# Kernel tuning notes

Measured on AMD Instinct MI355X. Metric: run time of the kernel, lower is better.

The kernel has to match this reference:

```python
import jax, jax.numpy as jnp
import numpy as np

EMBED = 1024
HEAD = 128

def setup_inputs() -> dict:
    key = jax.random.key(0)
    k1, k2, k3, k4 = jax.random.split(key, 4)
    x = jax.random.normal(k1, (8, 2048, EMBED), dtype=jnp.float32)
    s = 1.0 / np.sqrt(EMBED)
    Wk = jax.random.normal(k2, (EMBED, HEAD), dtype=jnp.float32) * s
    Wq = jax.random.normal(k3, (EMBED, HEAD), dtype=jnp.float32) * s
    Wv = jax.random.normal(k4, (EMBED, HEAD), dtype=jnp.float32) * s
    return {"x": x, "Wk": Wk, "Wq": Wq, "Wv": Wv}

def reference(x, Wk, Wq, Wv):
    # x: [B,T,E]; projections: [B,T,H]
    k = x @ Wk
    q = x @ Wq
    v = x @ Wv
    T = x.shape[1]
    # NOTE: original scales by 1/sqrt(embedding_size), not head_size
    scale = 1.0 / jnp.sqrt(jnp.asarray(EMBED, dtype=x.dtype))
    scores = jnp.einsum('bth,bsh->bts', q, k) * scale  # [B,T,T]
    causal = jnp.tril(jnp.ones((T, T), dtype=bool))
    scores = jnp.where(causal, scores, -jnp.inf)
    attn = jax.nn.softmax(scores, axis=-1)
    return jnp.einsum('bts,bsh->bth', attn, v)
```

## Files before the change

kernel.cpp:

```cpp
#include <hip/hip_runtime.h>
#include <math.h>

typedef short bf16x2 __attribute__((ext_vector_type(2)));
typedef short bf16x4 __attribute__((ext_vector_type(4)));
typedef short bf16x8 __attribute__((ext_vector_type(8)));
typedef float f32x4 __attribute__((ext_vector_type(4)));

#define EMBED 1024
#define HEAD 128
#define BATCH 8
#define SEQ 2048

__device__ __forceinline__ short f2bf(float f) {
  union { float f; unsigned u; } v;
  v.f = f;
  unsigned r = v.u + 0x7fffu + ((v.u >> 16) & 1u);
  return (short)(r >> 16);
}

__device__ __forceinline__ void async_copy16(const void* g, void* l) {
#if __has_builtin(__builtin_amdgcn_global_load_lds)
  __builtin_amdgcn_global_load_lds(
      (const __attribute__((address_space(1))) unsigned int*)g,
      (__attribute__((address_space(3))) unsigned int*)l, 16, 0, 0);
#else
  *(f32x4*)l = *(const f32x4*)g;
#endif
}

__global__ __launch_bounds__(256) void wtrans_kernel(
    const float* __restrict__ Wq, const float* __restrict__ Wk,
    const float* __restrict__ Wv, short* __restrict__ WT) {
  __shared__ float tile[32][33];
  int kt = blockIdx.x * 32;
  int ht = blockIdx.y * 32;
  int mtx = blockIdx.z;
  const float* W = (mtx == 0) ? Wq : ((mtx == 1) ? Wk : Wv);
  float scale = (mtx == 0) ? (1.4426950408889634f / 32.0f) : 1.0f;
  int tc = threadIdx.x & 31;
  int tr = threadIdx.x >> 5;
#pragma unroll
  for (int i = 0; i < 4; i++) {
    int r = tr + i * 8;
    tile[r][tc] = W[(size_t)(kt + r) * HEAD + ht + tc];
  }
  __syncthreads();
#pragma unroll
  for (int i = 0; i < 4; i++) {
    int r = tr + i * 8;
    WT[(size_t)(mtx * HEAD + ht + r) * EMBED + kt + tc] = f2bf(tile[tc][r] * scale);
  }
}

__global__ __launch_bounds__(512, 2) void proj_kernel(
    const float* __restrict__ x, const short* __restrict__ WT,
    short* __restrict__ q, short* __restrict__ k, short* __restrict__ vT) {
  __shared__ __align__(16) short As[2][64 * 72];
  __shared__ __align__(16) short Bs[2][3072 * 8];
  int tid = threadIdx.x;
  int w = tid >> 6, lane = tid & 63, quad = lane >> 4, sub = lane & 15;
  int mw = w & 1, nw = w >> 1;
  int mt = blockIdx.x;
  int m0 = mt * 64;
  int bb = m0 >> 11;
  int t0 = m0 & 2047;

  int arow = tid >> 3;
  int akq = (tid & 7) * 8;
  const float* xbase = x + (size_t)(m0 + arow) * EMBED + akq;
  int aoff = arow * 72 + akq;

  int kcg = tid >> 7;
  int n0 = tid & 127;
  const short* wsrc[6];
  int bdst[6];
#pragma unroll
  for (int j = 0; j < 3; j++)
#pragma unroll
    for (int kk = 0; kk < 2; kk++) {
      int kc = kcg * 2 + kk;
      int n = j * 128 + n0;
      wsrc[j * 2 + kk] = WT + (size_t)n * EMBED + kc * 8;
      bdst[j * 2 + kk] = (kc * 384 + n) * 8;
    }

  f32x4 acc[2][6];
#pragma unroll
  for (int am = 0; am < 2; am++)
#pragma unroll
    for (int an = 0; an < 6; an++) acc[am][an] = (f32x4)(0.0f);

  {
    f32x4 x0 = *(const f32x4*)(xbase + 0);
    f32x4 x1 = *(const f32x4*)(xbase + 4);
    bf16x8 w0;
    w0[0]=f2bf(x0[0]); w0[1]=f2bf(x0[1]); w0[2]=f2bf(x0[2]); w0[3]=f2bf(x0[3]);
    w0[4]=f2bf(x1[0]); w0[5]=f2bf(x1[1]); w0[6]=f2bf(x1[2]); w0[7]=f2bf(x1[3]);
    *(bf16x8*)&As[0][aoff] = w0;
#pragma unroll
    for (int j = 0; j < 6; j++) async_copy16(wsrc[j], &Bs[0][bdst[j]]);
  }
  f32x4 xr0 = *(const f32x4*)(xbase + 64);
  f32x4 xr1 = *(const f32x4*)(xbase + 68);

  for (int it = 0; it < 16; it++) {
    int cur = it & 1;
    __syncthreads();
    if (it < 15) {
      int nxt = cur ^ 1;
      bf16x8 w0;
      w0[0]=f2bf(xr0[0]); w0[1]=f2bf(xr0[1]); w0[2]=f2bf(xr0[2]); w0[3]=f2bf(xr0[3]);
      w0[4]=f2bf(xr1[0]); w0[5]=f2bf(xr1[1]); w0[6]=f2bf(xr1[2]); w0[7]=f2bf(xr1[3]);
      *(bf16x8*)&As[nxt][aoff] = w0;
      int kb1 = (it + 1) * 64;
#pragma unroll
      for (int j = 0; j < 6; j++)
        async_copy16(wsrc[j] + kb1, &Bs[nxt][bdst[j]]);
      if (it < 14) {
        int kb2 = (it + 2) * 64;
        xr0 = *(const f32x4*)(xbase + kb2);
        xr1 = *(const f32x4*)(xbase + kb2 + 4);
      }
    }
#pragma unroll
    for (int ks = 0; ks < 2; ks++) {
      bf16x8 a0 = *(const bf16x8*)&As[cur][(mw * 32 + sub) * 72 + ks * 32 + quad * 8];
      bf16x8 a1 = *(const bf16x8*)&As[cur][(mw * 32 + 16 + sub) * 72 + ks * 32 + quad * 8];
#pragma unroll
      for (int an = 0; an < 6; an++) {
        bf16x8 bf = *(const bf16x8*)&Bs[cur][((ks * 4 + quad) * 384 + nw * 96 + an * 16 + sub) * 8];
        acc[0][an] = __builtin_amdgcn_mfma_f32_16x16x32_bf16(a0, bf, acc[0][an], 0, 0, 0);
        acc[1][an] = __builtin_amdgcn_mfma_f32_16x16x32_bf16(a1, bf, acc[1][an], 0, 0, 0);
      }
    }
  }

  __syncthreads();
  short* vls = &As[0][0];
#pragma unroll
  for (int am = 0; am < 2; am++)
#pragma unroll
    for (int an = 0; an < 6; an++) {
      int g = nw * 6 + an;
      int mtx = g >> 3;
      int colm = (g & 7) * 16 + sub;
      if (mtx < 2) {
        short* dst = (mtx == 0) ? q : k;
#pragma unroll
        for (int r = 0; r < 4; r++) {
          int m = m0 + mw * 32 + am * 16 + quad * 4 + r;
          dst[(size_t)m * HEAD + colm] = f2bf(acc[am][an][r]);
        }
      } else {
        int mm = mw * 32 + am * 16 + quad * 4;
        bf16x4 pv;
#pragma unroll
        for (int r = 0; r < 4; r++) pv[r] = f2bf(acc[am][an][r]);
        *(bf16x4*)&vls[colm * 72 + mm] = pv;
      }
    }
  __syncthreads();
  int h = tid >> 2, seg = tid & 3;
  bf16x8 v0 = *(const bf16x8*)&vls[h * 72 + seg * 16];
  bf16x8 v1 = *(const bf16x8*)&vls[h * 72 + seg * 16 + 8];
  short* dp = vT + (size_t)(bb * HEAD + h) * SEQ + t0 + seg * 16;
  *(bf16x8*)(dp) = v0;
  *(bf16x8*)(dp + 8) = v1;
}

__global__ __launch_bounds__(256, 4) void attn_kernel(
    const short* __restrict__ q, const short* __restrict__ k,
    const short* __restrict__ vT, float* __restrict__ o_acc,
    float* __restrict__ l_acc) {
  __shared__ __align__(16) short Kb[2][4096];
  __shared__ __align__(16) short Vb[2][4096];
  __shared__ __align__(16) short Pb[4][2][16 * 40];
  int tid = threadIdx.x;
  int w = tid >> 6, lane = tid & 63, quad = lane >> 4, sub = lane & 15;
  int bx = blockIdx.x;
  int b = bx & 7;
  int v = 79 - (bx >> 3);
  int qt, c;
  if (v < 8)       { qt = v;                               c = 0; }
  else if (v < 24) { int i2 = v - 8;  qt = 8  + (i2 >> 1); c = i2 & 1; }
  else if (v < 48) { int i2 = v - 24; qt = 16 + i2 / 3;    c = i2 % 3; }
  else             { int i2 = v - 48; qt = 24 + (i2 >> 2); c = i2 & 3; }
  int q0 = qt * 64;
  int kb0 = c * 512;
  int len = min(512, q0 + 64 - kb0);
  int ntiles = len >> 5;

  const short* kp = k + (size_t)b * SEQ * HEAD;
  const short* vp = vT + (size_t)b * HEAD * SEQ;
  int cc0 = tid, cc1 = tid + 256;

  bf16x8 qf[4];
  const short* qrow = q + (size_t)(b * SEQ + q0 + w * 16 + sub) * HEAD + quad * 8;
#pragma unroll
  for (int kc = 0; kc < 4; kc++) qf[kc] = *(const bf16x8*)(qrow + kc * 32);

  f32x4 o[8];
#pragma unroll
  for (int h = 0; h < 8; h++) o[h] = (f32x4)(0.0f);
  float l[4] = {0.0f, 0.0f, 0.0f, 0.0f};
  int wrow = q0 + w * 16;
  int qrq = wrow + quad * 4;

  async_copy16(kp + (size_t)(kb0 + (cc0 & 31)) * HEAD + (cc0 >> 5) * 8, &Kb[0][cc0 * 8]);
  async_copy16(kp + (size_t)(kb0 + (cc1 & 31)) * HEAD + (cc1 >> 5) * 8, &Kb[0][cc1 * 8]);
  async_copy16(vp + (size_t)(cc0 & 127) * SEQ + kb0 + (cc0 >> 7) * 8, &Vb[0][cc0 * 8]);
  async_copy16(vp + (size_t)(cc1 & 127) * SEQ + kb0 + (cc1 >> 7) * 8, &Vb[0][cc1 * 8]);

  for (int j = 0; j < ntiles; j++) {
    int kb = kb0 + j * 32;
    int cur = j & 1;
    __syncthreads();
    if (j + 1 < ntiles) {
      int nxt = cur ^ 1;
      int kb1 = kb + 32;
      async_copy16(kp + (size_t)(kb1 + (cc0 & 31)) * HEAD + (cc0 >> 5) * 8, &Kb[nxt][cc0 * 8]);
      async_copy16(kp + (size_t)(kb1 + (cc1 & 31)) * HEAD + (cc1 >> 5) * 8, &Kb[nxt][cc1 * 8]);
      async_copy16(vp + (size_t)(cc0 & 127) * SEQ + kb1 + (cc0 >> 7) * 8, &Vb[nxt][cc0 * 8]);
      async_copy16(vp + (size_t)(cc1 & 127) * SEQ + kb1 + (cc1 >> 7) * 8, &Vb[nxt][cc1 * 8]);
    }
    f32x4 s0 = (f32x4)(0.0f), s1 = (f32x4)(0.0f);
#pragma unroll
    for (int kk = 0; kk < 4; kk++) {
      bf16x8 f0 = *(const bf16x8*)&Kb[cur][((kk * 4 + quad) * 32 + sub) * 8];
      bf16x8 f1 = *(const bf16x8*)&Kb[cur][((kk * 4 + quad) * 32 + 16 + sub) * 8];
      s0 = __builtin_amdgcn_mfma_f32_16x16x32_bf16(qf[kk], f0, s0, 0, 0, 0);
      s1 = __builtin_amdgcn_mfma_f32_16x16x32_bf16(qf[kk], f1, s1, 0, 0, 0);
    }
    bool edge = (kb + 31 > wrow);
    float e0[4], e1[4];
#pragma unroll
    for (int r = 0; r < 4; r++) {
      e0[r] = __builtin_amdgcn_exp2f(s0[r]);
      e1[r] = __builtin_amdgcn_exp2f(s1[r]);
    }
    if (edge) {
#pragma unroll
      for (int r = 0; r < 4; r++) {
        if (kb + sub > qrq + r) e0[r] = 0.0f;
        if (kb + 16 + sub > qrq + r) e1[r] = 0.0f;
      }
    }
    short* pw = &Pb[w][cur][0];
#pragma unroll
    for (int r = 0; r < 4; r++) {
      l[r] += e0[r] + e1[r];
      pw[(quad * 4 + r) * 40 + sub] = f2bf(e0[r]);
      pw[(quad * 4 + r) * 40 + sub + 16] = f2bf(e1[r]);
    }
    bf16x8 pa = *(const bf16x8*)&pw[sub * 40 + quad * 8];
#pragma unroll
    for (int h8 = 0; h8 < 8; h8++) {
      bf16x8 vf = *(const bf16x8*)&Vb[cur][(quad * 128 + h8 * 16 + sub) * 8];
      o[h8] = __builtin_amdgcn_mfma_f32_16x16x32_bf16(pa, vf, o[h8], 0, 0, 0);
    }
  }

  float* ob = o_acc + (size_t)(b * SEQ + qrq) * HEAD + sub;
#pragma unroll
  for (int r = 0; r < 4; r++)
#pragma unroll
    for (int h8 = 0; h8 < 8; h8++)
      unsafeAtomicAdd(ob + (size_t)r * HEAD + h8 * 16, o[h8][r]);
#pragma unroll
  for (int r = 0; r < 4; r++) {
#pragma unroll
    for (int off = 1; off < 16; off <<= 1) l[r] += __shfl_xor(l[r], off);
  }
  if (sub == 0) {
#pragma unroll
    for (int r = 0; r < 4; r++)
      unsafeAtomicAdd(&l_acc[b * SEQ + qrq + r], l[r]);
  }
}

__global__ __launch_bounds__(256) void norm_kernel(
    float* __restrict__ o, const float* __restrict__ l_acc) {
  int idx = blockIdx.x * 256 + threadIdx.x;
  f32x4 v = ((const f32x4*)o)[idx];
  float inv = 1.0f / l_acc[idx >> 5];
  v[0] *= inv; v[1] *= inv; v[2] *= inv; v[3] *= inv;
  ((f32x4*)o)[idx] = v;
}

extern "C" void kernel_launch(void* const* d_in, const int* in_sizes, int n_in,
                              void* d_out, int out_size, void* d_ws, size_t ws_size,
                              hipStream_t stream) {
  const float* x  = (const float*)d_in[0];
  const float* Wk = (const float*)d_in[1];
  const float* Wq = (const float*)d_in[2];
  const float* Wv = (const float*)d_in[3];
  char* ws = (char*)d_ws;
  short* WT    = (short*)(ws);
  short* vT    = (short*)(ws + (size_t)1  * (1 << 20));
  short* q     = (short*)(ws + (size_t)5  * (1 << 20));
  short* k     = (short*)(ws + (size_t)9  * (1 << 20));
  float* l_acc = (float*)(ws + (size_t)13 * (1 << 20));
  float* out   = (float*)d_out;

  hipMemsetAsync(out, 0, (size_t)BATCH * SEQ * HEAD * sizeof(float), stream);
  hipMemsetAsync(l_acc, 0, (size_t)BATCH * SEQ * sizeof(float), stream);
  wtrans_kernel<<<dim3(32, 4, 3), 256, 0, stream>>>(Wq, Wk, Wv, WT);
  proj_kernel<<<dim3(256), 512, 0, stream>>>(x, WT, q, k, vT);
  attn_kernel<<<dim3(640), 256, 0, stream>>>(q, k, vT, out, l_acc);
  norm_kernel<<<dim3(2048), 256, 0, stream>>>(out, l_acc);
}
```

Before: 175.6 us.

## Store weights, K and V in LDS-tile-ordered global layouts for contiguous async copies

The weight pre-pass now writes the bf16 weights already in the shared-memory tile order used by the projection kernel. The projection kernel writes K and V directly in 32-key tile blocks matching the attention kernel's LDS layout, which removes the LDS transpose and extra syncs for V. Each async copy in both kernels then reads a fully contiguous 8 KB block instead of strided rows. The cost is scattered 2-byte stores for K in the projection epilogue and a more specialised, harder-to-reuse intermediate layout.

Result: faster. 156.7 us (-10.8%).

```diff
diff --git a/kernel.cpp b/kernel.cpp
--- a/kernel.cpp
+++ b/kernel.cpp
@@ -28,42 +28,31 @@
 #endif
 }
 
-__global__ __launch_bounds__(256) void wtrans_kernel(
+__global__ __launch_bounds__(384) void wtrans_kernel(
     const float* __restrict__ Wq, const float* __restrict__ Wk,
-    const float* __restrict__ Wv, short* __restrict__ WT) {
-  __shared__ float tile[32][33];
-  int kt = blockIdx.x * 32;
-  int ht = blockIdx.y * 32;
-  int mtx = blockIdx.z;
+    const float* __restrict__ Wv, short* __restrict__ WT3) {
+  int kc8 = blockIdx.x;
+  int n = threadIdx.x;
+  int mtx = n >> 7, h = n & 127;
   const float* W = (mtx == 0) ? Wq : ((mtx == 1) ? Wk : Wv);
   float scale = (mtx == 0) ? (1.4426950408889634f / 32.0f) : 1.0f;
-  int tc = threadIdx.x & 31;
-  int tr = threadIdx.x >> 5;
-#pragma unroll
-  for (int i = 0; i < 4; i++) {
-    int r = tr + i * 8;
-    tile[r][tc] = W[(size_t)(kt + r) * HEAD + ht + tc];
-  }
-  __syncthreads();
-#pragma unroll
-  for (int i = 0; i < 4; i++) {
-    int r = tr + i * 8;
-    WT[(size_t)(mtx * HEAD + ht + r) * EMBED + kt + tc] = f2bf(tile[tc][r] * scale);
-  }
+  bf16x8 o;
+#pragma unroll
+  for (int j = 0; j < 8; j++)
+    o[j] = f2bf(W[(size_t)(kc8 * 8 + j) * HEAD + h] * scale);
+  *(bf16x8*)&WT3[(size_t)kc8 * 3072 + n * 8] = o;
 }
 
 __global__ __launch_bounds__(512, 2) void proj_kernel(
-    const float* __restrict__ x, const short* __restrict__ WT,
-    short* __restrict__ q, short* __restrict__ k, short* __restrict__ vT) {
+    const float* __restrict__ x, const short* __restrict__ WT3,
+    short* __restrict__ q, short* __restrict__ kG, short* __restrict__ vG) {
   __shared__ __align__(16) short As[2][64 * 72];
-  __shared__ __align__(16) short Bs[2][3072 * 8];
+  __shared__ __align__(16) short Bs[2][24576];
   int tid = threadIdx.x;
   int w = tid >> 6, lane = tid & 63, quad = lane >> 4, sub = lane & 15;
   int mw = w & 1, nw = w >> 1;
   int mt = blockIdx.x;
   int m0 = mt * 64;
-  int bb = m0 >> 11;
-  int t0 = m0 & 2047;
 
   int arow = tid >> 3;
   int akq = (tid & 7) * 8;
@@ -72,17 +61,12 @@
 
   int kcg = tid >> 7;
   int n0 = tid & 127;
-  const short* wsrc[6];
   int bdst[6];
 #pragma unroll
   for (int j = 0; j < 3; j++)
 #pragma unroll
-    for (int kk = 0; kk < 2; kk++) {
-      int kc = kcg * 2 + kk;
-      int n = j * 128 + n0;
-      wsrc[j * 2 + kk] = WT + (size_t)n * EMBED + kc * 8;
-      bdst[j * 2 + kk] = (kc * 384 + n) * 8;
-    }
+    for (int kk = 0; kk < 2; kk++)
+      bdst[j * 2 + kk] = ((kcg * 2 + kk) * 384 + j * 128 + n0) * 8;
 
   f32x4 acc[2][6];
 #pragma unroll
@@ -98,7 +82,7 @@
     w0[4]=f2bf(x1[0]); w0[5]=f2bf(x1[1]); w0[6]=f2bf(x1[2]); w0[7]=f2bf(x1[3]);
     *(bf16x8*)&As[0][aoff] = w0;
 #pragma unroll
-    for (int j = 0; j < 6; j++) async_copy16(wsrc[j], &Bs[0][bdst[j]]);
+    for (int j = 0; j < 6; j++) async_copy16(WT3 + bdst[j], &Bs[0][bdst[j]]);
   }
   f32x4 xr0 = *(const f32x4*)(xbase + 64);
   f32x4 xr1 = *(const f32x4*)(xbase + 68);
@@ -112,10 +96,10 @@
       w0[0]=f2bf(xr0[0]); w0[1]=f2bf(xr0[1]); w0[2]=f2bf(xr0[2]); w0[3]=f2bf(xr0[3]);
       w0[4]=f2bf(xr1[0]); w0[5]=f2bf(xr1[1]); w0[6]=f2bf(xr1[2]); w0[7]=f2bf(xr1[3]);
       *(bf16x8*)&As[nxt][aoff] = w0;
-      int kb1 = (it + 1) * 64;
+      int bsrc = (it + 1) * 24576;
 #pragma unroll
       for (int j = 0; j < 6; j++)
-        async_copy16(wsrc[j] + kb1, &Bs[nxt][bdst[j]]);
+        async_copy16(WT3 + bsrc + bdst[j], &Bs[nxt][bdst[j]]);
       if (it < 14) {
         int kb2 = (it + 2) * 64;
         xr0 = *(const f32x4*)(xbase + kb2);
@@ -135,42 +119,36 @@
     }
   }
 
-  __syncthreads();
-  short* vls = &As[0][0];
 #pragma unroll
   for (int am = 0; am < 2; am++)
 #pragma unroll
     for (int an = 0; an < 6; an++) {
       int g = nw * 6 + an;
-      int mtx = g >> 3;
-      int colm = (g & 7) * 16 + sub;
-      if (mtx < 2) {
-        short* dst = (mtx == 0) ? q : k;
+      int hcol = (g & 7) * 16 + sub;
+      if (g < 8) {
 #pragma unroll
         for (int r = 0; r < 4; r++) {
           int m = m0 + mw * 32 + am * 16 + quad * 4 + r;
-          dst[(size_t)m * HEAD + colm] = f2bf(acc[am][an][r]);
+          q[(size_t)m * HEAD + hcol] = f2bf(acc[am][an][r]);
         }
+      } else if (g < 16) {
+        size_t base = (size_t)(mt * 2 + mw) * 4096 + (hcol >> 3) * 256 + (hcol & 7);
+#pragma unroll
+        for (int r = 0; r < 4; r++)
+          kG[base + (am * 16 + quad * 4 + r) * 8] = f2bf(acc[am][an][r]);
       } else {
-        int mm = mw * 32 + am * 16 + quad * 4;
         bf16x4 pv;
 #pragma unroll
         for (int r = 0; r < 4; r++) pv[r] = f2bf(acc[am][an][r]);
-        *(bf16x4*)&vls[colm * 72 + mm] = pv;
-      }
-    }
-  __syncthreads();
-  int h = tid >> 2, seg = tid & 3;
-  bf16x8 v0 = *(const bf16x8*)&vls[h * 72 + seg * 16];
-  bf16x8 v1 = *(const bf16x8*)&vls[h * 72 + seg * 16 + 8];
-  short* dp = vT + (size_t)(bb * HEAD + h) * SEQ + t0 + seg * 16;
-  *(bf16x8*)(dp) = v0;
-  *(bf16x8*)(dp + 8) = v1;
+        *(bf16x4*)&vG[(size_t)(mt * 2 + mw) * 4096 + (am * 2 + (quad >> 1)) * 1024 +
+                      hcol * 8 + (quad & 1) * 4] = pv;
+      }
+    }
 }
 
 __global__ __launch_bounds__(256, 4) void attn_kernel(
-    const short* __restrict__ q, const short* __restrict__ k,
-    const short* __restrict__ vT, float* __restrict__ o_acc,
+    const short* __restrict__ q, const short* __restrict__ kG,
+    const short* __restrict__ vG, float* __restrict__ o_acc,
     float* __restrict__ l_acc) {
   __shared__ __align__(16) short Kb[2][4096];
   __shared__ __align__(16) short Vb[2][4096];
@@ -190,8 +168,8 @@
   int len = min(512, q0 + 64 - kb0);
   int ntiles = len >> 5;
 
-  const short* kp = k + (size_t)b * SEQ * HEAD;
-  const short* vp = vT + (size_t)b * HEAD * SEQ;
+  const short* kp = kG + (size_t)b * SEQ * HEAD;
+  const short* vp = vG + (size_t)b * SEQ * HEAD;
   int cc0 = tid, cc1 = tid + 256;
 
   bf16x8 qf[4];
@@ -206,10 +184,13 @@
   int wrow = q0 + w * 16;
   int qrq = wrow + quad * 4;
 
-  async_copy16(kp + (size_t)(kb0 + (cc0 & 31)) * HEAD + (cc0 >> 5) * 8, &Kb[0][cc0 * 8]);
-  async_copy16(kp + (size_t)(kb0 + (cc1 & 31)) * HEAD + (cc1 >> 5) * 8, &Kb[0][cc1 * 8]);
-  async_copy16(vp + (size_t)(cc0 & 127) * SEQ + kb0 + (cc0 >> 7) * 8, &Vb[0][cc0 * 8]);
-  async_copy16(vp + (size_t)(cc1 & 127) * SEQ + kb0 + (cc1 >> 7) * 8, &Vb[0][cc1 * 8]);
+  {
+    size_t blk = (size_t)(kb0 >> 5) * 4096;
+    async_copy16(kp + blk + cc0 * 8, &Kb[0][cc0 * 8]);
+    async_copy16(kp + blk + cc1 * 8, &Kb[0][cc1 * 8]);
+    async_copy16(vp + blk + cc0 * 8, &Vb[0][cc0 * 8]);
+    async_copy16(vp + blk + cc1 * 8, &Vb[0][cc1 * 8]);
+  }
 
   for (int j = 0; j < ntiles; j++) {
     int kb = kb0 + j * 32;
@@ -217,11 +198,11 @@
     __syncthreads();
     if (j + 1 < ntiles) {
       int nxt = cur ^ 1;
-      int kb1 = kb + 32;
-      async_copy16(kp + (size_t)(kb1 + (cc0 & 31)) * HEAD + (cc0 >> 5) * 8, &Kb[nxt][cc0 * 8]);
-      async_copy16(kp + (size_t)(kb1 + (cc1 & 31)) * HEAD + (cc1 >> 5) * 8, &Kb[nxt][cc1 * 8]);
-      async_copy16(vp + (size_t)(cc0 & 127) * SEQ + kb1 + (cc0 >> 7) * 8, &Vb[nxt][cc0 * 8]);
-      async_copy16(vp + (size_t)(cc1 & 127) * SEQ + kb1 + (cc1 >> 7) * 8, &Vb[nxt][cc1 * 8]);
+      size_t blk = (size_t)((kb + 32) >> 5) * 4096;
+      async_copy16(kp + blk + cc0 * 8, &Kb[nxt][cc0 * 8]);
+      async_copy16(kp + blk + cc1 * 8, &Kb[nxt][cc1 * 8]);
+      async_copy16(vp + blk + cc0 * 8, &Vb[nxt][cc0 * 8]);
+      async_copy16(vp + blk + cc1 * 8, &Vb[nxt][cc1 * 8]);
     }
     f32x4 s0 = (f32x4)(0.0f), s1 = (f32x4)(0.0f);
 #pragma unroll
@@ -295,17 +276,17 @@
   const float* Wq = (const float*)d_in[2];
   const float* Wv = (const float*)d_in[3];
   char* ws = (char*)d_ws;
-  short* WT    = (short*)(ws);
-  short* vT    = (short*)(ws + (size_t)1  * (1 << 20));
+  short* WT3   = (short*)(ws);
+  short* vG    = (short*)(ws + (size_t)1  * (1 << 20));
   short* q     = (short*)(ws + (size_t)5  * (1 << 20));
-  short* k     = (short*)(ws + (size_t)9  * (1 << 20));
+  short* kG    = (short*)(ws + (size_t)9  * (1 << 20));
   float* l_acc = (float*)(ws + (size_t)13 * (1 << 20));
   float* out   = (float*)d_out;
 
   hipMemsetAsync(out, 0, (size_t)BATCH * SEQ * HEAD * sizeof(float), stream);
   hipMemsetAsync(l_acc, 0, (size_t)BATCH * SEQ * sizeof(float), stream);
-  wtrans_kernel<<<dim3(32, 4, 3), 256, 0, stream>>>(Wq, Wk, Wv, WT);
-  proj_kernel<<<dim3(256), 512, 0, stream>>>(x, WT, q, k, vT);
-  attn_kernel<<<dim3(640), 256, 0, stream>>>(q, k, vT, out, l_acc);
+  wtrans_kernel<<<dim3(128), 384, 0, stream>>>(Wq, Wk, Wv, WT3);
+  proj_kernel<<<dim3(256), 512, 0, stream>>>(x, WT3, q, kG, vG);
+  attn_kernel<<<dim3(640), 256, 0, stream>>>(q, kG, vG, out, l_acc);
   norm_kernel<<<dim3(2048), 256, 0, stream>>>(out, l_acc);
 }
```
